# Optimization experiments

Measured on AMD Instinct MI355X. Metric: run time of the kernel, lower is better.

## Reference

```python
import jax, jax.numpy as jnp
import numpy as np

NV, NC, E = 100000, 50000, 800000
VD, CD, H, ROUNDS = 4, 1, 128, 2


def _ln(x, g, b):
    mu = jnp.mean(x, axis=-1, keepdims=True)
    v = jnp.mean((x - mu) ** 2, axis=-1, keepdims=True)
    return (x - mu) * jax.lax.rsqrt(v + 1e-5) * g + b


def _agg(msg, dst, n):
    # degree-normalized scatter-add: out[v] = sum_{e: dst[e]=v} msg[e] / (deg(v)+1e-6)
    s = jax.ops.segment_sum(msg, dst, num_segments=n)
    cnt = jax.ops.segment_sum(jnp.ones((msg.shape[0],), msg.dtype), dst, num_segments=n)
    return s / (cnt[:, None] + 1e-6)


def setup_inputs() -> dict:
    key = jax.random.key(0)
    ks = jax.random.split(key, 16)
    p = lambda k, sh: jax.random.normal(k, sh, jnp.float32) * 0.05
    z = lambda: jnp.zeros((H,), jnp.float32)
    o = lambda: jnp.ones((H,), jnp.float32)
    return {
        'x_var': jax.random.normal(ks[0], (NV, VD), jnp.float32),
        'x_con': jax.random.normal(ks[1], (NC, CD), jnp.float32),
        'e_vc_src': jax.random.randint(ks[2], (E,), 0, NV, jnp.int32),
        'e_vc_dst': jax.random.randint(ks[3], (E,), 0, NC, jnp.int32),
        'e_cv_src': jax.random.randint(ks[4], (E,), 0, NC, jnp.int32),
        'e_cv_dst': jax.random.randint(ks[5], (E,), 0, NV, jnp.int32),
        'var_proj_w': p(ks[6], (VD, H)), 'var_proj_b': z(),
        'con_proj_w': p(ks[7], (CD, H)), 'con_proj_b': z(),
        'v2c_msg_w': p(ks[8], (H, H)), 'v2c_msg_b': z(),
        'v2c_upd_w': p(ks[9], (H + 1, H)), 'v2c_upd_b': z(),
        'v2c_ln_g': o(), 'v2c_ln_b': z(),
        'c2v_msg_w': p(ks[10], (H, H)), 'c2v_msg_b': z(),
        'c2v_ln_g': o(), 'c2v_ln_b': z(),
        'var_gate_w': p(ks[11], (2 * H, H)), 'var_gate_b': z(),
        'con_gate_w': p(ks[12], (2 * H, H)), 'con_gate_b': z(),
        'var_ln_g': o(), 'var_ln_b': z(),
        'con_ln_g': o(), 'con_ln_b': z(),
    }


def reference(x_var, x_con, e_vc_src, e_vc_dst, e_cv_src, e_cv_dst,
              var_proj_w, var_proj_b, con_proj_w, con_proj_b,
              v2c_msg_w, v2c_msg_b, v2c_upd_w, v2c_upd_b, v2c_ln_g, v2c_ln_b,
              c2v_msg_w, c2v_msg_b, c2v_ln_g, c2v_ln_b,
              var_gate_w, var_gate_b, con_gate_w, con_gate_b,
              var_ln_g, var_ln_b, con_ln_g, con_ln_b):
    clue = x_con[:, 0]  # (NC,)
    hv = _ln(jax.nn.relu(x_var @ var_proj_w + var_proj_b), var_ln_g, var_ln_b)  # (NV,H)
    hc = _ln(jax.nn.relu(x_con @ con_proj_w + con_proj_b), con_ln_g, con_ln_b)  # (NC,H)
    for _ in range(ROUNDS):
        # var -> con
        msg = hv[e_vc_src] @ v2c_msg_w + v2c_msg_b  # (E,H)
        agg = _agg(msg, e_vc_dst, NC)
        upd = jnp.concatenate([agg, clue[:, None]], axis=1)  # (NC,H+1)
        con_new = _ln(jax.nn.relu(upd @ v2c_upd_w + v2c_upd_b), v2c_ln_g, v2c_ln_b)
        g = jax.nn.sigmoid(jnp.concatenate([hc, con_new], axis=1) @ con_gate_w + con_gate_b)
        hc = g * con_new + (1 - g) * hc
        # con -> var
        msg2 = hc[e_cv_src] @ c2v_msg_w + c2v_msg_b  # (E,H)
        var_new = _ln(jax.nn.relu(_agg(msg2, e_cv_dst, NV)), c2v_ln_g, c2v_ln_b)
        g2 = jax.nn.sigmoid(jnp.concatenate([hv, var_new], axis=1) @ var_gate_w + var_gate_b)
        hv = g2 * var_new + (1 - g2) * hv
    return hv
```

## Files before the change

kernel.cpp:

```cpp
#include <hip/hip_runtime.h>
#include <stdint.h>

#define NVN 100000
#define NCN 50000
#define NE  800000
#define H   128

typedef __attribute__((ext_vector_type(8))) short bf16x8;
typedef __attribute__((ext_vector_type(4))) float f32x4;

static __device__ __forceinline__ float wredsum(float v) {
#pragma unroll
  for (int off = 32; off > 0; off >>= 1) v += __shfl_xor(v, off, 64);
  return v;
}
static __device__ __forceinline__ float sigmoidf(float x) { return 1.0f / (1.0f + __expf(-x)); }
static __device__ __forceinline__ unsigned short f2bf(float f) {
  unsigned int u = __float_as_uint(f);
  return (unsigned short)((u + 0x7FFFu + ((u >> 16) & 1u)) >> 16);
}
static __device__ __forceinline__ short2 splitbf(float f) {
  unsigned short h = f2bf(f);
  float hf = __uint_as_float(((unsigned int)h) << 16);
  short2 r;
  r.x = (short)h;
  r.y = (short)f2bf(f - hf);
  return r;
}

__global__ __launch_bounds__(256) void k_init_var(const float* __restrict__ xv,
    const float* __restrict__ w, const float* __restrict__ b,
    const float* __restrict__ g, const float* __restrict__ bb,
    float* __restrict__ hv, unsigned short* __restrict__ hb) {
  int wid = (blockIdx.x * 256 + threadIdx.x) >> 6;
  int lane = threadIdx.x & 63;
  if (wid >= NVN) return;
  float x0 = xv[wid*4+0], x1 = xv[wid*4+1], x2 = xv[wid*4+2], x3 = xv[wid*4+3];
  int c0 = lane, c1 = lane + 64;
  float v0 = b[c0] + x0*w[c0] + x1*w[H+c0] + x2*w[2*H+c0] + x3*w[3*H+c0];
  float v1 = b[c1] + x0*w[c1] + x1*w[H+c1] + x2*w[2*H+c1] + x3*w[3*H+c1];
  v0 = fmaxf(v0, 0.f); v1 = fmaxf(v1, 0.f);
  float mu = wredsum(v0 + v1) * (1.0f/H);
  float d0 = v0 - mu, d1 = v1 - mu;
  float var = wredsum(d0*d0 + d1*d1) * (1.0f/H);
  float r = rsqrtf(var + 1e-5f);
  float o0 = d0*r*g[c0] + bb[c0], o1 = d1*r*g[c1] + bb[c1];
  hv[(size_t)wid*H + c0] = o0;  hv[(size_t)wid*H + c1] = o1;
  hb[(size_t)wid*H + c0] = f2bf(o0);  hb[(size_t)wid*H + c1] = f2bf(o1);
}

__global__ __launch_bounds__(256) void k_init_con(const float* __restrict__ xc,
    const float* __restrict__ w, const float* __restrict__ b,
    const float* __restrict__ g, const float* __restrict__ bb,
    float* __restrict__ hc, unsigned short* __restrict__ hb) {
  int wid = (blockIdx.x * 256 + threadIdx.x) >> 6;
  int lane = threadIdx.x & 63;
  if (wid >= NCN) return;
  float x = xc[wid];
  int c0 = lane, c1 = lane + 64;
  float v0 = fmaxf(b[c0] + x*w[c0], 0.f);
  float v1 = fmaxf(b[c1] + x*w[c1], 0.f);
  float mu = wredsum(v0 + v1) * (1.0f/H);
  float d0 = v0 - mu, d1 = v1 - mu;
  float var = wredsum(d0*d0 + d1*d1) * (1.0f/H);
  float r = rsqrtf(var + 1e-5f);
  float o0 = d0*r*g[c0] + bb[c0], o1 = d1*r*g[c1] + bb[c1];
  hc[(size_t)wid*H + c0] = o0;  hc[(size_t)wid*H + c1] = o1;
  hb[(size_t)wid*H + c0] = f2bf(o0);  hb[(size_t)wid*H + c1] = f2bf(o1);
}

__global__ void k_fuse_w(const float* __restrict__ wm, const float* __restrict__ wu,
                         float* __restrict__ wf) {
  int idx = blockIdx.x*256 + threadIdx.x;
  int i = idx >> 7, j = idx & 127;
  float a = 0.f;
  for (int k = 0; k < H; ++k) a = fmaf(wm[i*H+k], wu[k*H+j], a);
  wf[idx] = a;
}
__global__ void k_fuse_b(const float* __restrict__ bm, const float* __restrict__ wu,
                         float* __restrict__ bf) {
  int j = threadIdx.x;
  float a = 0.f;
  for (int k = 0; k < H; ++k) a = fmaf(bm[k], wu[k*H+j], a);
  bf[j] = a;
}

__global__ __launch_bounds__(256) void k_perm2(const float* __restrict__ W,
    unsigned short* __restrict__ Whi, unsigned short* __restrict__ Wlo, int K) {
  int idx = blockIdx.x*256 + threadIdx.x;
  if (idx >= K*H) return;
  int j = idx & 7, lane = (idx >> 3) & 63, ct = (idx >> 9) & 7, kb = idx >> 12;
  int k = kb*32 + (lane >> 4)*8 + j, c = ct*16 + (lane & 15);
  float w = W[k*H + c];
  unsigned short h = f2bf(w);
  float hf = __uint_as_float(((unsigned int)h) << 16);
  Whi[idx] = h;
  Wlo[idx] = f2bf(w - hf);
}

__global__ void k_count(const int* __restrict__ dc, const int* __restrict__ dv,
                        int* __restrict__ cnt_c, int* __restrict__ cnt_v) {
  for (int e = blockIdx.x*blockDim.x + threadIdx.x; e < NE; e += gridDim.x*blockDim.x) {
    atomicAdd(&cnt_c[dc[e]], 1);
    atomicAdd(&cnt_v[dv[e]], 1);
  }
}
__global__ __launch_bounds__(256) void k_scan1(const int* __restrict__ in, int* __restrict__ out,
                                               int* __restrict__ aux, int n) {
  __shared__ int s[256];
  int t = threadIdx.x, i = blockIdx.x*256 + t;
  int v = (i < n) ? in[i] : 0;
  s[t] = v; __syncthreads();
  for (int off = 1; off < 256; off <<= 1) {
    int x = (t >= off) ? s[t - off] : 0;
    __syncthreads();
    s[t] += x;
    __syncthreads();
  }
  if (i < n) out[i] = s[t] - v;
  if (t == 255) aux[blockIdx.x] = s[255];
}
__global__ __launch_bounds__(1024) void k_scan2(int* __restrict__ aux, int nb) {
  __shared__ int s[1024];
  int t = threadIdx.x;
  int v = (t < nb) ? aux[t] : 0;
  s[t] = v; __syncthreads();
  for (int off = 1; off < 1024; off <<= 1) {
    int x = (t >= off) ? s[t-off] : 0;
    __syncthreads();
    s[t] += x;
    __syncthreads();
  }
  if (t < nb) aux[t] = s[t] - v;
}
__global__ __launch_bounds__(256) void k_scan3(int* __restrict__ out, const int* __restrict__ aux,
                                               int n, int total) {
  int i = blockIdx.x*256 + threadIdx.x;
  if (i < n) out[i] += aux[blockIdx.x];
  if (i == 0) out[n] = total;
}
__global__ void k_scatter(const int* __restrict__ sc, const int* __restrict__ dc,
                          const int* __restrict__ sv, const int* __restrict__ dv,
                          const int* __restrict__ off_c, int* __restrict__ cur_c, int* __restrict__ lst_c,
                          const int* __restrict__ off_v, int* __restrict__ cur_v, int* __restrict__ lst_v) {
  for (int e = blockIdx.x*blockDim.x + threadIdx.x; e < NE; e += gridDim.x*blockDim.x) {
    int d = dc[e]; int p = atomicAdd(&cur_c[d], 1); (void)atomicExch(&lst_c[off_c[d] + p], sc[e]);
    d = dv[e];     p = atomicAdd(&cur_v[d], 1);     (void)atomicExch(&lst_v[off_v[d] + p], sv[e]);
  }
}

__global__ __launch_bounds__(256) void k_gather_bf(const unsigned int* __restrict__ tab,
    const int* __restrict__ off, const int* __restrict__ lst,
    float* __restrict__ out, int n) {
  int wid = (blockIdx.x * 256 + threadIdx.x) >> 6;
  int lane = threadIdx.x & 63;
  if (wid >= n) return;
  int s0 = off[wid], s1 = off[wid+1];
  const int grp = lane >> 4, c16 = lane & 15;
  float acc[8];
#pragma unroll
  for (int j = 0; j < 8; ++j) acc[j] = 0.f;
#pragma unroll 2
  for (int p = s0 + grp; p < s1; p += 4) {
    int idx = lst[p];
    uint4 u = *(const uint4*)(tab + (size_t)idx*64 + c16*4);
    acc[0] += __uint_as_float(u.x << 16);
    acc[1] += __uint_as_float(u.x & 0xFFFF0000u);
    acc[2] += __uint_as_float(u.y << 16);
    acc[3] += __uint_as_float(u.y & 0xFFFF0000u);
    acc[4] += __uint_as_float(u.z << 16);
    acc[5] += __uint_as_float(u.z & 0xFFFF0000u);
    acc[6] += __uint_as_float(u.w << 16);
    acc[7] += __uint_as_float(u.w & 0xFFFF0000u);
  }
#pragma unroll
  for (int j = 0; j < 8; ++j) {
    acc[j] += __shfl_xor(acc[j], 16, 64);
    acc[j] += __shfl_xor(acc[j], 32, 64);
  }
  if (lane < 16) {
    float inv = 1.0f / ((float)(s1 - s0) + 1e-6f);
    float* op = out + (size_t)wid*H + c16*8;
    *(float4*)(op)     = make_float4(acc[0]*inv, acc[1]*inv, acc[2]*inv, acc[3]*inv);
    *(float4*)(op + 4) = make_float4(acc[4]*inv, acc[5]*inv, acc[6]*inv, acc[7]*inv);
  }
}

template<int EPI>
__global__ __launch_bounds__(128) void k_mleg(
    const float* __restrict__ A,
    const unsigned short* __restrict__ Wph, const unsigned short* __restrict__ Wpl,
    const int* __restrict__ cnt, const float* __restrict__ xc,
    const float* __restrict__ vb, const float* __restrict__ wcl,
    const float* __restrict__ badd, const float* __restrict__ lng,
    const float* __restrict__ lnb,
    const unsigned short* __restrict__ Gph, const float* __restrict__ gb,
    float* __restrict__ Hm, unsigned short* __restrict__ Hb, int n) {
  __shared__ float lds[32][132];
  const int wv = threadIdx.x >> 6, lane = threadIdx.x & 63;
  const int rbase = blockIdx.x*32 + wv*16;
  if (rbase >= n) return;
  const int g = lane >> 4, c15 = lane & 15;
  int arow = rbase + c15; if (arow > n-1) arow = n-1;

  const float* Ar1 = Hm + (size_t)arow*H + g*8;
  float4 pf[8];
#pragma unroll
  for (int kb = 0; kb < 4; ++kb) {
    pf[2*kb]   = *(const float4*)(Ar1 + kb*32);
    pf[2*kb+1] = *(const float4*)(Ar1 + kb*32 + 4);
  }

  {
    const float* Ar = A + (size_t)arow*H + g*8;
    bf16x8 ahi[4], alo[4];
#pragma unroll
    for (int kb = 0; kb < 4; ++kb) {
      float4 p0 = *(const float4*)(Ar + kb*32);
      float4 p1 = *(const float4*)(Ar + kb*32 + 4);
      bf16x8 h, l;
      short2 s;
      s = splitbf(p0.x); h[0] = s.x; l[0] = s.y;
      s = splitbf(p0.y); h[1] = s.x; l[1] = s.y;
      s = splitbf(p0.z); h[2] = s.x; l[2] = s.y;
      s = splitbf(p0.w); h[3] = s.x; l[3] = s.y;
      s = splitbf(p1.x); h[4] = s.x; l[4] = s.y;
      s = splitbf(p1.y); h[5] = s.x; l[5] = s.y;
      s = splitbf(p1.z); h[6] = s.x; l[6] = s.y;
      s = splitbf(p1.w); h[7] = s.x; l[7] = s.y;
      ahi[kb] = h; alo[kb] = l;
    }
    const bf16x8* Bph = (const bf16x8*)Wph;
    const bf16x8* Bpl = (const bf16x8*)Wpl;
    f32x4 zero = {0.f, 0.f, 0.f, 0.f};
    f32x4 acc[8];
#pragma unroll
    for (int ct = 0; ct < 8; ++ct) acc[ct] = zero;
#pragma unroll
    for (int kb = 0; kb < 4; ++kb)
#pragma unroll
      for (int ct = 0; ct < 8; ++ct) {
        bf16x8 bh = Bph[(kb*8+ct)*64 + lane];
        bf16x8 bl = Bpl[(kb*8+ct)*64 + lane];
        acc[ct] = __builtin_amdgcn_mfma_f32_16x16x32_bf16(ahi[kb], bh, acc[ct], 0, 0, 0);
        acc[ct] = __builtin_amdgcn_mfma_f32_16x16x32_bf16(alo[kb], bh, acc[ct], 0, 0, 0);
        acc[ct] = __builtin_amdgcn_mfma_f32_16x16x32_bf16(ahi[kb], bl, acc[ct], 0, 0, 0);
      }
#pragma unroll
    for (int r = 0; r < 4; ++r)
#pragma unroll
      for (int ct = 0; ct < 8; ++ct)
        lds[wv*16 + g*4 + r][ct*16 + c15] = acc[ct][r];
  }

  {
    float vb0 = vb[lane], vb1 = vb[lane+64];
    float lg0 = lng[lane], lg1 = lng[lane+64];
    float lb0 = lnb[lane], lb1 = lnb[lane+64];
    float wc0 = 0.f, wc1 = 0.f, ba0 = 0.f, ba1 = 0.f;
    if constexpr (EPI == 0) {
      wc0 = wcl[lane]; wc1 = wcl[lane+64];
      ba0 = badd[lane]; ba1 = badd[lane+64];
    }
    auto lnrow = [&](int row, int dst) {
      float cf = (float)cnt[dst];
      float scale = cf / (cf + 1e-6f);
      float v0 = lds[row][lane]     + scale*vb0;
      float v1 = lds[row][lane+64]  + scale*vb1;
      if constexpr (EPI == 0) {
        float clue = xc[dst];
        v0 += clue*wc0 + ba0;
        v1 += clue*wc1 + ba1;
      }
      v0 = fmaxf(v0, 0.f); v1 = fmaxf(v1, 0.f);
      float mu = wredsum(v0 + v1) * (1.0f/H);
      float d0 = v0 - mu, d1 = v1 - mu;
      float var = wredsum(d0*d0 + d1*d1) * (1.0f/H);
      float r = rsqrtf(var + 1e-5f);
      lds[row][lane]      = d0*r*lg0 + lb0;
      lds[row][lane + 64] = d1*r*lg1 + lb1;
    };
    const int blk = blockIdx.x*32;
    if (blk + 32 <= n) {
#pragma unroll
      for (int i = 0; i < 16; ++i) lnrow(wv*16 + i, blk + wv*16 + i);
    } else {
      for (int i = 0; i < 16; ++i) {
        int dst = blk + wv*16 + i;
        if (dst >= n) break;
        lnrow(wv*16 + i, dst);
      }
    }
  }

  {
    bf16x8 ahi[8], alo[8];
#pragma unroll
    for (int kb = 0; kb < 4; ++kb) {
      float4 p0 = pf[2*kb];
      float4 p1 = pf[2*kb+1];
      bf16x8 h, l;
      short2 s;
      s = splitbf(p0.x); h[0] = s.x; l[0] = s.y;
      s = splitbf(p0.y); h[1] = s.x; l[1] = s.y;
      s = splitbf(p0.z); h[2] = s.x; l[2] = s.y;
      s = splitbf(p0.w); h[3] = s.x; l[3] = s.y;
      s = splitbf(p1.x); h[4] = s.x; l[4] = s.y;
      s = splitbf(p1.y); h[5] = s.x; l[5] = s.y;
      s = splitbf(p1.z); h[6] = s.x; l[6] = s.y;
      s = splitbf(p1.w); h[7] = s.x; l[7] = s.y;
      ahi[kb] = h; alo[kb] = l;
    }
    const float* Ar2 = &lds[wv*16 + c15][0];
#pragma unroll
    for (int kb = 4; kb < 8; ++kb) {
      float4 p0 = *(const float4*)(Ar2 + (kb-4)*32 + g*8);
      float4 p1 = *(const float4*)(Ar2 + (kb-4)*32 + g*8 + 4);
      bf16x8 h, l;
      short2 s;
      s = splitbf(p0.x); h[0] = s.x; l[0] = s.y;
      s = splitbf(p0.y); h[1] = s.x; l[1] = s.y;
      s = splitbf(p0.z); h[2] = s.x; l[2] = s.y;
      s = splitbf(p0.w); h[3] = s.x; l[3] = s.y;
      s = splitbf(p1.x); h[4] = s.x; l[4] = s.y;
      s = splitbf(p1.y); h[5] = s.x; l[5] = s.y;
      s = splitbf(p1.z); h[6] = s.x; l[6] = s.y;
      s = splitbf(p1.w); h[7] = s.x; l[7] = s.y;
      ahi[kb] = h; alo[kb] = l;
    }
    const bf16x8* Bph = (const bf16x8*)Gph;
    f32x4 zero = {0.f, 0.f, 0.f, 0.f};
    f32x4 acc[8];
#pragma unroll
    for (int ct = 0; ct < 8; ++ct) acc[ct] = zero;
#pragma unroll
    for (int kb = 0; kb < 8; ++kb)
#pragma unroll
      for (int ct = 0; ct < 8; ++ct) {
        bf16x8 bh = Bph[(kb*8+ct)*64 + lane];
        acc[ct] = __builtin_amdgcn_mfma_f32_16x16x32_bf16(ahi[kb], bh, acc[ct], 0, 0, 0);
        acc[ct] = __builtin_amdgcn_mfma_f32_16x16x32_bf16(alo[kb], bh, acc[ct], 0, 0, 0);
      }
    float gbv[8];
#pragma unroll
    for (int ct = 0; ct < 8; ++ct) gbv[ct] = gb[ct*16 + c15];
#pragma unroll
    for (int r = 0; r < 4; ++r) {
      int rg = rbase + g*4 + r;
      if (rg >= n) continue;
      int row = wv*16 + g*4 + r;
      float* hp = Hm + (size_t)rg*H + c15;
      unsigned short* hbp = Hb + (size_t)rg*H + c15;
#pragma unroll
      for (int ct = 0; ct < 8; ++ct) {
        float gg = sigmoidf(acc[ct][r] + gbv[ct]);
        float nv = lds[row][ct*16 + c15];
        float ov = hp[ct*16];
        float res = gg*nv + (1.f - gg)*ov;
        hp[ct*16] = res;
        hbp[ct*16] = f2bf(res);
      }
    }
  }
}

extern "C" void kernel_launch(void* const* d_in, const int* in_sizes, int n_in,
                              void* d_out, int out_size, void* d_ws, size_t ws_size,
                              hipStream_t stream) {
  const float* x_var   = (const float*)d_in[0];
  const float* x_con   = (const float*)d_in[1];
  const int*   evc_src = (const int*)d_in[2];
  const int*   evc_dst = (const int*)d_in[3];
  const int*   ecv_src = (const int*)d_in[4];
  const int*   ecv_dst = (const int*)d_in[5];
  const float* vproj_w = (const float*)d_in[6];
  const float* vproj_b = (const float*)d_in[7];
  const float* cproj_w = (const float*)d_in[8];
  const float* cproj_b = (const float*)d_in[9];
  const float* wmsg    = (const float*)d_in[10];
  const float* bmsg    = (const float*)d_in[11];
  const float* wupd    = (const float*)d_in[12];
  const float* bupd    = (const float*)d_in[13];
  const float* v2c_ln_g = (const float*)d_in[14];
  const float* v2c_ln_b = (const float*)d_in[15];
  const float* wc2v    = (const float*)d_in[16];
  const float* bc2v    = (const float*)d_in[17];
  const float* c2v_ln_g = (const float*)d_in[18];
  const float* c2v_ln_b = (const float*)d_in[19];
  const float* vgate_w = (const float*)d_in[20];
  const float* vgate_b = (const float*)d_in[21];
  const float* cgate_w = (const float*)d_in[22];
  const float* cgate_b = (const float*)d_in[23];
  const float* var_ln_g = (const float*)d_in[24];
  const float* var_ln_b = (const float*)d_in[25];
  const float* con_ln_g = (const float*)d_in[26];
  const float* con_ln_b = (const float*)d_in[27];
  float* hv = (float*)d_out;

  char* p = (char*)d_ws;
  auto carve = [&](size_t bytes) { char* r = p; p += (bytes + 255) & ~(size_t)255; return r; };
  int* cnt_c = (int*)carve((size_t)NCN*4);
  int* cur_c = (int*)carve((size_t)NCN*4);
  int* cnt_v = (int*)carve((size_t)NVN*4);
  int* cur_v = (int*)carve((size_t)NVN*4);
  int* off_c = (int*)carve((size_t)(NCN+1)*4);
  int* off_v = (int*)carve((size_t)(NVN+1)*4);
  int* aux   = (int*)carve(1024*4);
  int* lst_c = (int*)carve((size_t)NE*4);
  int* lst_v = (int*)carve((size_t)NE*4);
  float* wf  = (float*)carve((size_t)H*H*4);
  float* bfu = (float*)carve((size_t)H*4);
  unsigned short* wfph = (unsigned short*)carve((size_t)H*H*2);
  unsigned short* wfpl = (unsigned short*)carve((size_t)H*H*2);
  unsigned short* wvph = (unsigned short*)carve((size_t)H*H*2);
  unsigned short* wvpl = (unsigned short*)carve((size_t)H*H*2);
  unsigned short* cgph = (unsigned short*)carve((size_t)2*H*H*2);
  unsigned short* cgpl = (unsigned short*)carve((size_t)2*H*H*2);
  unsigned short* vgph = (unsigned short*)carve((size_t)2*H*H*2);
  unsigned short* vgpl = (unsigned short*)carve((size_t)2*H*H*2);
  float* hc    = (float*)carve((size_t)NCN*H*4);
  float* t_c   = (float*)carve((size_t)NCN*H*4);
  float* t_v   = (float*)carve((size_t)NVN*H*4);
  unsigned short* hvb = (unsigned short*)carve((size_t)NVN*H*2);
  unsigned short* hcb = (unsigned short*)carve((size_t)NCN*H*2);
  if ((size_t)(p - (char*)d_ws) > ws_size) return;

  (void)hipMemsetAsync(cnt_c, 0, (size_t)NCN*4, stream);
  (void)hipMemsetAsync(cur_c, 0, (size_t)NCN*4, stream);
  (void)hipMemsetAsync(cnt_v, 0, (size_t)NVN*4, stream);
  (void)hipMemsetAsync(cur_v, 0, (size_t)NVN*4, stream);

  k_fuse_w<<<64, 256, 0, stream>>>(wmsg, wupd, wf);
  k_fuse_b<<<1, 128, 0, stream>>>(bmsg, wupd, bfu);
  k_perm2<<<(H*H+255)/256, 256, 0, stream>>>(wf, wfph, wfpl, H);
  k_perm2<<<(H*H+255)/256, 256, 0, stream>>>(wc2v, wvph, wvpl, H);
  k_perm2<<<(2*H*H+255)/256, 256, 0, stream>>>(cgate_w, cgph, cgpl, 2*H);
  k_perm2<<<(2*H*H+255)/256, 256, 0, stream>>>(vgate_w, vgph, vgpl, 2*H);

  k_count<<<2048, 256, 0, stream>>>(evc_dst, ecv_dst, cnt_c, cnt_v);
  int nbc = (NCN + 255)/256, nbv = (NVN + 255)/256;
  k_scan1<<<nbc, 256, 0, stream>>>(cnt_c, off_c, aux, NCN);
  k_scan2<<<1, 1024, 0, stream>>>(aux, nbc);
  k_scan3<<<nbc, 256, 0, stream>>>(off_c, aux, NCN, NE);
  k_scan1<<<nbv, 256, 0, stream>>>(cnt_v, off_v, aux, NVN);
  k_scan2<<<1, 1024, 0, stream>>>(aux, nbv);
  k_scan3<<<nbv, 256, 0, stream>>>(off_v, aux, NVN, NE);
  k_scatter<<<2048, 256, 0, stream>>>(evc_src, evc_dst, ecv_src, ecv_dst,
                                      off_c, cur_c, lst_c, off_v, cur_v, lst_v);

  k_init_var<<<NVN/4, 256, 0, stream>>>(x_var, vproj_w, vproj_b, var_ln_g, var_ln_b, hv, hvb);
  k_init_con<<<NCN/4, 256, 0, stream>>>(x_con, cproj_w, cproj_b, con_ln_g, con_ln_b, hc, hcb);

  for (int r = 0; r < 2; ++r) {
    k_gather_bf<<<(NCN+3)/4, 256, 0, stream>>>((const unsigned int*)hvb, off_c, lst_c, t_c, NCN);
    k_mleg<0><<<(NCN+31)/32, 128, 0, stream>>>(t_c, wfph, wfpl, cnt_c, x_con, bfu, wupd + H*H,
                                               bupd, v2c_ln_g, v2c_ln_b, cgph, cgate_b,
                                               hc, hcb, NCN);
    k_gather_bf<<<(NVN+3)/4, 256, 0, stream>>>((const unsigned int*)hcb, off_v, lst_v, t_v, NVN);
    k_mleg<1><<<(NVN+31)/32, 128, 0, stream>>>(t_v, wvph, wvpl, cnt_v, nullptr, bc2v, nullptr,
                                               nullptr, c2v_ln_g, c2v_ln_b, vgph, vgate_b,
                                               hv, hvb, NVN);
  }
}
```

Before: 624.0 us.

## Batch gather index loads, merge scan launches, and reuse counts as scatter cursors

Result: no change. 622.5 us (-0.2%).

```diff
diff --git a/kernel.cpp b/kernel.cpp
--- a/kernel.cpp
+++ b/kernel.cpp
@@ -105,10 +105,15 @@
     atomicAdd(&cnt_v[dv[e]], 1);
   }
 }
-__global__ __launch_bounds__(256) void k_scan1(const int* __restrict__ in, int* __restrict__ out,
-                                               int* __restrict__ aux, int n) {
+__global__ __launch_bounds__(256) void k_scan1m(
+    const int* __restrict__ in_c, int* __restrict__ out_c, int* __restrict__ aux_c, int nbc, int n_c,
+    const int* __restrict__ in_v, int* __restrict__ out_v, int* __restrict__ aux_v, int n_v) {
+  const int b = blockIdx.x;
+  const int* in; int* out; int* aux; int n; int lb;
+  if (b < nbc) { in = in_c; out = out_c; aux = aux_c; n = n_c; lb = b; }
+  else         { in = in_v; out = out_v; aux = aux_v; n = n_v; lb = b - nbc; }
   __shared__ int s[256];
-  int t = threadIdx.x, i = blockIdx.x*256 + t;
+  int t = threadIdx.x, i = lb*256 + t;
   int v = (i < n) ? in[i] : 0;
   s[t] = v; __syncthreads();
   for (int off = 1; off < 256; off <<= 1) {
@@ -118,9 +123,12 @@
     __syncthreads();
   }
   if (i < n) out[i] = s[t] - v;
-  if (t == 255) aux[blockIdx.x] = s[255];
-}
-__global__ __launch_bounds__(1024) void k_scan2(int* __restrict__ aux, int nb) {
+  if (t == 255) aux[lb] = s[255];
+}
+__global__ __launch_bounds__(1024) void k_scan2m(int* __restrict__ aux_c, int nbc,
+                                                 int* __restrict__ aux_v, int nbv) {
+  int* aux = (blockIdx.x == 0) ? aux_c : aux_v;
+  int nb   = (blockIdx.x == 0) ? nbc : nbv;
   __shared__ int s[1024];
   int t = threadIdx.x;
   int v = (t < nb) ? aux[t] : 0;
@@ -133,45 +141,65 @@
   }
   if (t < nb) aux[t] = s[t] - v;
 }
-__global__ __launch_bounds__(256) void k_scan3(int* __restrict__ out, const int* __restrict__ aux,
-                                               int n, int total) {
-  int i = blockIdx.x*256 + threadIdx.x;
-  if (i < n) out[i] += aux[blockIdx.x];
+__global__ __launch_bounds__(256) void k_scan3m(
+    int* __restrict__ out_c, const int* __restrict__ aux_c, int nbc, int n_c,
+    int* __restrict__ out_v, const int* __restrict__ aux_v, int n_v, int total) {
+  const int b = blockIdx.x;
+  int* out; const int* aux; int n; int lb;
+  if (b < nbc) { out = out_c; aux = aux_c; n = n_c; lb = b; }
+  else         { out = out_v; aux = aux_v; n = n_v; lb = b - nbc; }
+  int i = lb*256 + threadIdx.x;
+  if (i < n) out[i] += aux[lb];
   if (i == 0) out[n] = total;
 }
 __global__ void k_scatter(const int* __restrict__ sc, const int* __restrict__ dc,
                           const int* __restrict__ sv, const int* __restrict__ dv,
-                          const int* __restrict__ off_c, int* __restrict__ cur_c, int* __restrict__ lst_c,
-                          const int* __restrict__ off_v, int* __restrict__ cur_v, int* __restrict__ lst_v) {
+                          const int* __restrict__ off_c, int* __restrict__ cnt_c, int* __restrict__ lst_c,
+                          const int* __restrict__ off_v, int* __restrict__ cnt_v, int* __restrict__ lst_v) {
   for (int e = blockIdx.x*blockDim.x + threadIdx.x; e < NE; e += gridDim.x*blockDim.x) {
-    int d = dc[e]; int p = atomicAdd(&cur_c[d], 1); (void)atomicExch(&lst_c[off_c[d] + p], sc[e]);
-    d = dv[e];     p = atomicAdd(&cur_v[d], 1);     (void)atomicExch(&lst_v[off_v[d] + p], sv[e]);
+    int d = dc[e]; int p = atomicSub(&cnt_c[d], 1) - 1; lst_c[off_c[d] + p] = sc[e];
+    d = dv[e];     p = atomicSub(&cnt_v[d], 1) - 1;     lst_v[off_v[d] + p] = sv[e];
   }
 }
 
 __global__ __launch_bounds__(256) void k_gather_bf(const unsigned int* __restrict__ tab,
     const int* __restrict__ off, const int* __restrict__ lst,
-    float* __restrict__ out, int n) {
+    float* __restrict__ out, int n, int tabn) {
   int wid = (blockIdx.x * 256 + threadIdx.x) >> 6;
   int lane = threadIdx.x & 63;
   if (wid >= n) return;
   int s0 = off[wid], s1 = off[wid+1];
   const int grp = lane >> 4, c16 = lane & 15;
+  int pl = (s1 - 1 < s0) ? s0 : s1 - 1;
+  if (pl >= NE) pl = NE - 1;
   float acc[8];
 #pragma unroll
   for (int j = 0; j < 8; ++j) acc[j] = 0.f;
-#pragma unroll 2
-  for (int p = s0 + grp; p < s1; p += 4) {
-    int idx = lst[p];
-    uint4 u = *(const uint4*)(tab + (size_t)idx*64 + c16*4);
-    acc[0] += __uint_as_float(u.x << 16);
-    acc[1] += __uint_as_float(u.x & 0xFFFF0000u);
-    acc[2] += __uint_as_float(u.y << 16);
-    acc[3] += __uint_as_float(u.y & 0xFFFF0000u);
-    acc[4] += __uint_as_float(u.z << 16);
-    acc[5] += __uint_as_float(u.z & 0xFFFF0000u);
-    acc[6] += __uint_as_float(u.w << 16);
-    acc[7] += __uint_as_float(u.w & 0xFFFF0000u);
+  for (int base = s0; base < s1; base += 32) {
+    int idxs[8];
+    float msk[8];
+#pragma unroll
+    for (int j = 0; j < 8; ++j) {
+      int p = base + grp + 4*j;
+      msk[j] = (p < s1) ? 1.f : 0.f;
+      int pc = (p < s1) ? p : pl;
+      int ix = lst[pc];
+      ix = ix < 0 ? 0 : (ix >= tabn ? tabn - 1 : ix);
+      idxs[j] = ix;
+    }
+#pragma unroll
+    for (int j = 0; j < 8; ++j) {
+      uint4 u = *(const uint4*)(tab + (size_t)idxs[j]*64 + c16*4);
+      float m = msk[j];
+      acc[0] = fmaf(m, __uint_as_float(u.x << 16),          acc[0]);
+      acc[1] = fmaf(m, __uint_as_float(u.x & 0xFFFF0000u),  acc[1]);
+      acc[2] = fmaf(m, __uint_as_float(u.y << 16),          acc[2]);
+      acc[3] = fmaf(m, __uint_as_float(u.y & 0xFFFF0000u),  acc[3]);
+      acc[4] = fmaf(m, __uint_as_float(u.z << 16),          acc[4]);
+      acc[5] = fmaf(m, __uint_as_float(u.z & 0xFFFF0000u),  acc[5]);
+      acc[6] = fmaf(m, __uint_as_float(u.w << 16),          acc[6]);
+      acc[7] = fmaf(m, __uint_as_float(u.w & 0xFFFF0000u),  acc[7]);
+    }
   }
 #pragma unroll
   for (int j = 0; j < 8; ++j) {
@@ -190,7 +218,7 @@
 __global__ __launch_bounds__(128) void k_mleg(
     const float* __restrict__ A,
     const unsigned short* __restrict__ Wph, const unsigned short* __restrict__ Wpl,
-    const int* __restrict__ cnt, const float* __restrict__ xc,
+    const int* __restrict__ off, const float* __restrict__ xc,
     const float* __restrict__ vb, const float* __restrict__ wcl,
     const float* __restrict__ badd, const float* __restrict__ lng,
     const float* __restrict__ lnb,
@@ -263,7 +291,7 @@
       ba0 = badd[lane]; ba1 = badd[lane+64];
     }
     auto lnrow = [&](int row, int dst) {
-      float cf = (float)cnt[dst];
+      float cf = (float)(off[dst+1] - off[dst]);
       float scale = cf / (cf + 1e-6f);
       float v0 = lds[row][lane]     + scale*vb0;
       float v1 = lds[row][lane+64]  + scale*vb1;
@@ -400,12 +428,11 @@
   char* p = (char*)d_ws;
   auto carve = [&](size_t bytes) { char* r = p; p += (bytes + 255) & ~(size_t)255; return r; };
   int* cnt_c = (int*)carve((size_t)NCN*4);
-  int* cur_c = (int*)carve((size_t)NCN*4);
   int* cnt_v = (int*)carve((size_t)NVN*4);
-  int* cur_v = (int*)carve((size_t)NVN*4);
   int* off_c = (int*)carve((size_t)(NCN+1)*4);
   int* off_v = (int*)carve((size_t)(NVN+1)*4);
-  int* aux   = (int*)carve(1024*4);
+  int* aux_c = (int*)carve(1024*4);
+  int* aux_v = (int*)carve(1024*4);
   int* lst_c = (int*)carve((size_t)NE*4);
   int* lst_v = (int*)carve((size_t)NE*4);
   float* wf  = (float*)carve((size_t)H*H*4);
@@ -426,9 +453,7 @@
   if ((size_t)(p - (char*)d_ws) > ws_size) return;
 
   (void)hipMemsetAsync(cnt_c, 0, (size_t)NCN*4, stream);
-  (void)hipMemsetAsync(cur_c, 0, (size_t)NCN*4, stream);
   (void)hipMemsetAsync(cnt_v, 0, (size_t)NVN*4, stream);
-  (void)hipMemsetAsync(cur_v, 0, (size_t)NVN*4, stream);
 
   k_fuse_w<<<64, 256, 0, stream>>>(wmsg, wupd, wf);
   k_fuse_b<<<1, 128, 0, stream>>>(bmsg, wupd, bfu);
@@ -439,25 +464,26 @@
 
   k_count<<<2048, 256, 0, stream>>>(evc_dst, ecv_dst, cnt_c, cnt_v);
   int nbc = (NCN + 255)/256, nbv = (NVN + 255)/256;
-  k_scan1<<<nbc, 256, 0, stream>>>(cnt_c, off_c, aux, NCN);
-  k_scan2<<<1, 1024, 0, stream>>>(aux, nbc);
-  k_scan3<<<nbc, 256, 0, stream>>>(off_c, aux, NCN, NE);
-  k_scan1<<<nbv, 256, 0, stream>>>(cnt_v, off_v, aux, NVN);
-  k_scan2<<<1, 1024, 0, stream>>>(aux, nbv);
-  k_scan3<<<nbv, 256, 0, stream>>>(off_v, aux, NVN, NE);
+  k_scan1m<<<nbc + nbv, 256, 0, stream>>>(cnt_c, off_c, aux_c, nbc, NCN,
+                                          cnt_v, off_v, aux_v, NVN);
+  k_scan2m<<<2, 1024, 0, stream>>>(aux_c, nbc, aux_v, nbv);
+  k_scan3m<<<nbc + nbv, 256, 0, stream>>>(off_c, aux_c, nbc, NCN,
+                                          off_v, aux_v, NVN, NE);
   k_scatter<<<2048, 256, 0, stream>>>(evc_src, evc_dst, ecv_src, ecv_dst,
-                                      off_c, cur_c, lst_c, off_v, cur_v, lst_v);
+                                      off_c, cnt_c, lst_c, off_v, cnt_v, lst_v);
 
   k_init_var<<<NVN/4, 256, 0, stream>>>(x_var, vproj_w, vproj_b, var_ln_g, var_ln_b, hv, hvb);
   k_init_con<<<NCN/4, 256, 0, stream>>>(x_con, cproj_w, cproj_b, con_ln_g, con_ln_b, hc, hcb);
 
   for (int r = 0; r < 2; ++r) {
-    k_gather_bf<<<(NCN+3)/4, 256, 0, stream>>>((const unsigned int*)hvb, off_c, lst_c, t_c, NCN);
-    k_mleg<0><<<(NCN+31)/32, 128, 0, stream>>>(t_c, wfph, wfpl, cnt_c, x_con, bfu, wupd + H*H,
+    k_gather_bf<<<(NCN+3)/4, 256, 0, stream>>>((const unsigned int*)hvb, off_c, lst_c,
+                                               t_c, NCN, NVN);
+    k_mleg<0><<<(NCN+31)/32, 128, 0, stream>>>(t_c, wfph, wfpl, off_c, x_con, bfu, wupd + H*H,
                                                bupd, v2c_ln_g, v2c_ln_b, cgph, cgate_b,
                                                hc, hcb, NCN);
-    k_gather_bf<<<(NVN+3)/4, 256, 0, stream>>>((const unsigned int*)hcb, off_v, lst_v, t_v, NVN);
-    k_mleg<1><<<(NVN+31)/32, 128, 0, stream>>>(t_v, wvph, wvpl, cnt_v, nullptr, bc2v, nullptr,
+    k_gather_bf<<<(NVN+3)/4, 256, 0, stream>>>((const unsigned int*)hcb, off_v, lst_v,
+                                               t_v, NVN, NCN);
+    k_mleg<1><<<(NVN+31)/32, 128, 0, stream>>>(t_v, wvph, wvpl, off_v, nullptr, bc2v, nullptr,
                                                nullptr, c2v_ln_g, c2v_ln_b, vgph, vgate_b,
                                                hv, hvb, NVN);
   }
```
